# Kernel tuning notes

Hardware: AMD Instinct MI355X
Metric: run time of the kernel (lower is better)

Reference implementation:

```python
import jax, jax.numpy as jnp
import numpy as np

N_E = 1024
E_DIM = 256
BETA = 0.25
PERSISTENCE = 0.1
B, T = 16, 1024


def setup_inputs() -> dict:
    key = jax.random.key(0)
    k1, k2 = jax.random.split(key)
    z = jax.random.normal(k1, (B, T, E_DIM), dtype=jnp.float32)
    # nn.Embedding(1+n_e, e_dim) init uniform(-1/n_e, 1/n_e)
    emb_weight = jax.random.uniform(k2, (N_E + 1, E_DIM), dtype=jnp.float32,
                                    minval=-1.0 / N_E, maxval=1.0 / N_E)
    return {"z": z, "emb_weight": emb_weight}


def _loss_contrast(z, ind, book):
    # z: (B,T,e), ind: (B,T) int, book: (n_e+1, e)
    z_q = book[ind]                                   # (B,T,e)
    loss_indices = jnp.sum((z - z_q) ** 2, axis=-1)   # (B,T)
    # ||z - book||^2 expanded to avoid the (B,T,n_e+1,e) intermediate
    z_sq = jnp.sum(z * z, axis=-1)                    # (B,T)
    b_sq = jnp.sum(book * book, axis=-1)              # (n_e+1,)
    cross = jnp.einsum('bte,ne->btn', z, book)        # (B,T,n_e+1)
    loss_all = z_sq[..., None] + b_sq[None, None, :] - 2.0 * cross
    lc = jnp.maximum(loss_indices[..., None] - loss_all + 1e-6 / N_E, 0.0)
    return jnp.mean(lc)


def _forward(z, emb_weight):
    zf = z.reshape(-1, E_DIM)
    d = (jnp.sum(zf * zf, axis=1, keepdims=True)
         + jnp.sum(emb_weight * emb_weight, axis=1)
         - 2.0 * (zf @ emb_weight.T)).reshape(B, T, N_E + 1)

    ind0 = jnp.clip(jnp.argmin(d[:, 0, :], axis=1), 0, N_E - 1)  # (B,)

    def step(carry, d_t):
        ind, coe = carry                              # (B,) int, (B,) f32
        d_here = jnp.take_along_axis(d_t, ind[:, None], axis=1)[:, 0]
        ind_next = jnp.minimum(ind + 1, N_E - 1)
        d_next = jnp.take_along_axis(d_t, ind_next[:, None], axis=1)[:, 0]
        stay = d_here <= d_next - coe
        ind_new = jnp.where(stay, ind, ind_next)
        coe_new = jnp.where(stay, coe + PERSISTENCE / N_E, 0.0)
        return (ind_new, coe_new), ind_new

    coe0 = jnp.zeros((B,), jnp.float32)
    _, inds = jax.lax.scan(step, (ind0, coe0), jnp.swapaxes(d[:, 1:, :], 0, 1))
    encoding_indices = jnp.concatenate([ind0[None, :], inds], axis=0).T  # (B,T)

    book_sg = jax.lax.stop_gradient(emb_weight)  # torch uses .data/.detach() everywhere
    z_q_raw = book_sg[encoding_indices]
    z_q = z + jax.lax.stop_gradient(z_q_raw - z)  # straight-through

    # non-legacy: beta * L(z, sg(book)) + L(sg(z), sg(book))
    loss = (BETA * _loss_contrast(z, encoding_indices, book_sg)
            + _loss_contrast(jax.lax.stop_gradient(z), encoding_indices, book_sg))

    v = jnp.max(encoding_indices) - jnp.min(encoding_indices)
    return z_q, loss, encoding_indices, v


def reference(z, emb_weight):
    return _forward(z, emb_weight)
```

## Files before the change

kernel.cpp:

```cpp
#include <hip/hip_runtime.h>

#define N_E   1024
#define EDIM  256
#define BB    16
#define TT    1024
#define NROW  (BB*TT)
#define NCOL  1025
#define NPAD  1152
#define PERS  (0.1f/1024.0f)
#define EPSC  (1e-6f/1024.0f)

#define OUT_LOSS 4194304
#define OUT_IDX  4194305
#define OUT_V    4210689

#define WS_ZB   0ull
#define WS_BBF  8388608ull
#define WS_BSQ  8978432ull
#define WS_E    8983552ull
#define WS_IND  84481024ull
#define WS_PART 84546560ull

typedef __attribute__((ext_vector_type(8))) short short8;
typedef __attribute__((ext_vector_type(4))) float floatx4;

__device__ __forceinline__ unsigned short f2bf(float f) {
    unsigned int u = __float_as_uint(f);
    u = (u + 0x7fffu + ((u >> 16) & 1u)) >> 16;
    return (unsigned short)u;
}

__device__ __forceinline__ float gload_f32(const float* p) {
    float r;
    asm volatile("global_load_dword %0, %1, off" : "=v"(r) : "v"(p));
    return r;
}

__global__ __launch_bounds__(256) void k0_prep(const float* __restrict__ z,
                                               const float* __restrict__ book,
                                               unsigned short* __restrict__ zb,
                                               unsigned short* __restrict__ bb,
                                               float* __restrict__ bsq) {
    int bx = blockIdx.x, tid = threadIdx.x;
    if (bx < 4096) {
        float4 v = ((const float4*)z)[bx * 256 + tid];
        size_t o = ((size_t)bx * 256 + tid) * 4;
        zb[o + 0] = f2bf(v.x); zb[o + 1] = f2bf(v.y);
        zb[o + 2] = f2bf(v.z); zb[o + 3] = f2bf(v.w);
    } else {
        int row = bx - 4096;
        float v = (row < NCOL) ? book[(size_t)row * EDIM + tid] : 0.0f;
        bb[(size_t)row * EDIM + tid] = f2bf(v);
        __shared__ float sd[256];
        sd[tid] = v * v;
        __syncthreads();
        for (int s = 128; s > 0; s >>= 1) { if (tid < s) sd[tid] += sd[tid + s]; __syncthreads(); }
        if (tid == 0) bsq[row] = sd[0];
    }
}

__global__ __launch_bounds__(256) void k1_gemm(const unsigned short* __restrict__ zb,
                                               const unsigned short* __restrict__ bb,
                                               const float* __restrict__ bsq,
                                               float* __restrict__ e) {
    int tid = threadIdx.x;
    int lane = tid & 63, w = tid >> 6;
    int mBase = blockIdx.x * 128 + (w >> 1) * 64;
    int nBase = blockIdx.y * 128 + (w & 1) * 64;
    int r = lane & 15, q = lane >> 4;

    floatx4 acc[4][4];
    #pragma unroll
    for (int i = 0; i < 4; i++)
        #pragma unroll
        for (int j = 0; j < 4; j++) acc[i][j] = (floatx4){0.f, 0.f, 0.f, 0.f};

    const short8* A = (const short8*)zb;
    const short8* Bm = (const short8*)bb;

    #pragma unroll
    for (int ks = 0; ks < 8; ks++) {
        int k8 = ks * 4 + q;
        short8 a[4], b[4];
        #pragma unroll
        for (int i = 0; i < 4; i++) a[i] = A[(size_t)(mBase + i * 16 + r) * 32 + k8];
        #pragma unroll
        for (int j = 0; j < 4; j++) b[j] = Bm[(size_t)(nBase + j * 16 + r) * 32 + k8];
        #pragma unroll
        for (int i = 0; i < 4; i++)
            #pragma unroll
            for (int j = 0; j < 4; j++)
                acc[i][j] = __builtin_amdgcn_mfma_f32_16x16x32_bf16(a[i], b[j], acc[i][j], 0, 0, 0);
    }

    float bsql[4];
    #pragma unroll
    for (int j = 0; j < 4; j++) bsql[j] = bsq[nBase + j * 16 + r];

    #pragma unroll
    for (int i = 0; i < 4; i++)
        #pragma unroll
        for (int rr = 0; rr < 4; rr++) {
            int m = mBase + i * 16 + q * 4 + rr;
            float* erow = e + (size_t)m * NPAD;
            #pragma unroll
            for (int j = 0; j < 4; j++)
                erow[nBase + j * 16 + r] = fmaf(-2.0f, acc[i][j][rr], bsql[j]);
        }
}

__global__ __launch_bounds__(256, 1) void k2_scan(const float* __restrict__ z,
                                                  const float* __restrict__ book,
                                                  const float* __restrict__ bsq,
                                                  const float* __restrict__ e,
                                                  int* __restrict__ wind) {
    __shared__ float sb[4]; __shared__ int si[4];

    int b = blockIdx.x, tid = threadIdx.x;
    int lane = tid & 63, w = tid >> 6;

    const float4* zr = (const float4*)(z + (size_t)b * TT * EDIM);
    float4 zv = zr[lane];
    float s = zv.x * zv.x + zv.y * zv.y + zv.z * zv.z + zv.w * zv.w;
    #pragma unroll
    for (int off = 32; off; off >>= 1) s += __shfl_xor(s, off, 64);
    float zsq = s;

    float best = 3.4e38f; int bidx = 0;
    for (int wi = w; wi < 17; wi += 4) {
        int n = wi * 64 + lane;
        if (n < NCOL) {
            const float4* br = (const float4*)(book + (size_t)n * EDIM);
            float c0 = 0.f, c1 = 0.f, c2 = 0.f, c3 = 0.f;
            #pragma unroll 8
            for (int k = 0; k < 64; k++) {
                float4 bo = br[k]; float4 za = zr[k];
                c0 = fmaf(za.x, bo.x, c0); c1 = fmaf(za.y, bo.y, c1);
                c2 = fmaf(za.z, bo.z, c2); c3 = fmaf(za.w, bo.w, c3);
            }
            float cr = (c0 + c1) + (c2 + c3);
            float d0 = (zsq + bsq[n]) - 2.0f * cr;
            if (d0 < best || (d0 == best && n < bidx)) { best = d0; bidx = n; }
        }
    }
    #pragma unroll
    for (int off = 32; off; off >>= 1) {
        float ob = __shfl_xor(best, off, 64);
        int   oi = __shfl_xor(bidx, off, 64);
        if (ob < best || (ob == best && oi < bidx)) { best = ob; bidx = oi; }
    }
    if (lane == 0) { sb[w] = best; si[w] = bidx; }
    __syncthreads();
    if (w != 0) return;

    best = sb[0]; bidx = si[0];
    for (int i = 1; i < 4; i++) {
        float vv = sb[i]; int ii = si[i];
        if (vv < best || (vv == best && ii < bidx)) { best = vv; bidx = ii; }
    }

    int ind = min(bidx, N_E - 1);
    int kk = 0;
    size_t ibase = (size_t)b * TT;
    if (lane == 0) wind[ibase] = ind;

    const float* eb = e + (size_t)b * TT * NPAD;
    const float QS = 1.0f / PERS;

    float a[31];
    int   q[31];

    int cb = min(ind, 960);
    {
        #pragma unroll
        for (int j = 0; j < 31; j++)
            a[j] = gload_f32(eb + (size_t)(1 + j) * NPAD + cb + lane);
        asm volatile("s_waitcnt vmcnt(0)" ::: "memory");
        __builtin_amdgcn_sched_barrier(0);
        bool cap = (cb + lane == 1023);
        #pragma unroll
        for (int j = 0; j < 31; j++) {
            float bv = __shfl_down(a[j], 1, 64);
            int qv = (int)((bv - a[j]) * QS);
            q[j] = cap ? 0 : qv;
        }
    }

    int t = 1;
    #pragma unroll 1
    for (int c = 0; c < 33; c++) {
        int cbn = min(ind, 960);
        #pragma unroll
        for (int j = 0; j < 31; j++) {
            int tn = t + 31 + j; tn = tn < 1024 ? tn : 1023;
            a[j] = gload_f32(eb + (size_t)tn * NPAD + cbn + lane);
        }
        __builtin_amdgcn_sched_barrier(0);

        int packed = 0;
        #pragma unroll
        for (int j = 0; j < 31; j++) {
            int rel = ind - cb;
            int qv = __builtin_amdgcn_readlane(q[j], rel);
            bool stay = (kk <= qv);
            int ip1 = ind + 1; ip1 = ip1 < 1023 ? ip1 : 1023;
            ind = stay ? ind : ip1;
            kk  = stay ? kk + 1 : 0;
            packed = (lane == j) ? ind : packed;
        }
        if (lane < 31) wind[ibase + t + lane] = packed;
        __builtin_amdgcn_sched_barrier(0);

        asm volatile("s_waitcnt vmcnt(0)" ::: "memory");
        __builtin_amdgcn_sched_barrier(0);
        bool cap = (cbn + lane == 1023);
        #pragma unroll
        for (int j = 0; j < 31; j++) {
            float bv = __shfl_down(a[j], 1, 64);
            int qv = (int)((bv - a[j]) * QS);
            q[j] = cap ? 0 : qv;
        }
        cb = cbn;
        t += 31;
    }
}

__global__ __launch_bounds__(256) void k3_loss_zq(const float* __restrict__ e,
                                                  const int* __restrict__ wind,
                                                  const float* __restrict__ book,
                                                  float* __restrict__ part,
                                                  float* __restrict__ out) {
    int rIdx = blockIdx.x, tid = threadIdx.x;
    int ind = wind[rIdx];
    const float* er = e + (size_t)rIdx * NPAD;
    float eind = er[ind];
    float p = 0.0f;
    for (int n = tid; n < NCOL; n += 256) {
        float v = eind - er[n] + EPSC;
        p += v > 0.0f ? v : 0.0f;
    }
    __shared__ float sd[256];
    sd[tid] = p; __syncthreads();
    for (int s = 128; s > 0; s >>= 1) { if (tid < s) sd[tid] += sd[tid + s]; __syncthreads(); }
    if (tid == 0) { part[rIdx] = sd[0]; out[OUT_IDX + rIdx] = (float)ind; }
    out[(size_t)rIdx * 256 + tid] = book[(size_t)ind * EDIM + tid];
}

__global__ __launch_bounds__(256) void k4_final(const float* __restrict__ part,
                                                const int* __restrict__ wind,
                                                float* __restrict__ out) {
    int tid = threadIdx.x;
    float s = 0.0f;
    for (int i = tid; i < NROW; i += 256) s += part[i];
    __shared__ float sd[256];
    sd[tid] = s; __syncthreads();
    for (int st = 128; st > 0; st >>= 1) { if (tid < st) sd[tid] += sd[tid + st]; __syncthreads(); }
    if (tid == 0) {
        int mn = wind[0], mx = wind[TT - 1];
        for (int b = 1; b < BB; b++) {
            mn = min(mn, wind[(size_t)b * TT]);
            mx = max(mx, wind[(size_t)b * TT + TT - 1]);
        }
        out[OUT_LOSS] = 1.25f * sd[0] / ((float)NROW * (float)NCOL);
        out[OUT_V] = (float)(mx - mn);
    }
}

extern "C" void kernel_launch(void* const* d_in, const int* in_sizes, int n_in,
                              void* d_out, int out_size, void* d_ws, size_t ws_size,
                              hipStream_t stream) {
    const float* z    = (const float*)d_in[0];
    const float* book = (const float*)d_in[1];
    char* ws = (char*)d_ws;
    unsigned short* zb = (unsigned short*)(ws + WS_ZB);
    unsigned short* bb = (unsigned short*)(ws + WS_BBF);
    float* bsq  = (float*)(ws + WS_BSQ);
    float* e    = (float*)(ws + WS_E);
    int*   wind = (int*)(ws + WS_IND);
    float* part = (float*)(ws + WS_PART);
    float* out  = (float*)d_out;

    hipLaunchKernelGGL(k0_prep,    dim3(4096 + 1152), dim3(256), 0, stream, z, book, zb, bb, bsq);
    hipLaunchKernelGGL(k1_gemm,    dim3(128, 9),      dim3(256), 0, stream, zb, bb, bsq, e);
    hipLaunchKernelGGL(k2_scan,    dim3(16),          dim3(256), 0, stream, z, book, bsq, e, wind);
    hipLaunchKernelGGL(k3_loss_zq, dim3(16384),       dim3(256), 0, stream, e, wind, book, part, out);
    hipLaunchKernelGGL(k4_final,   dim3(1),           dim3(256), 0, stream, part, wind, out);
}
```

Baseline: 256.6 us.

## Triple-buffer scan prefetch with 15-step chunks and partial vmcnt waits

Restructures the sequential scan kernel's prefetch of distance rows from a single 31-row buffer with a full vmcnt(0) wait into three rotating 15-row register buffers. Loads are issued two chunks ahead and only the oldest batch is waited on via vmcnt(31). The aim is to hide global-load latency behind the serial index-update chain. In exchange the scan advances 15 steps per chunk, so there are more iterations, and the prefetch column base is chosen from an index that is further out of date. Correctness depends on the index not drifting more than 63 columns within the lookahead window.

```diff
diff --git a/kernel.cpp b/kernel.cpp
--- a/kernel.cpp
+++ b/kernel.cpp
@@ -109,6 +109,46 @@
         }
 }
 
+
+#define R15(X) X(0) X(1) X(2) X(3) X(4) X(5) X(6) X(7) X(8) X(9) X(10) X(11) X(12) X(13) X(14)
+
+#define DECLA(i) float A0_##i, A1_##i, A2_##i; int q_##i;
+
+#define LDR(S,i) { int _t = _tb + i; _t = _t < 1024 ? _t : 1023; \
+                   A##S##_##i = gload_f32(_pe + (size_t)_t * NPAD); }
+#define LD0(i) LDR(0,i)
+#define LD1(i) LDR(1,i)
+#define LD2(i) LDR(2,i)
+
+#define QC(S,i) { float _bv = __shfl_down(A##S##_##i, 1, 64); \
+                  int _qv = (int)((_bv - A##S##_##i) * QS); \
+                  q_##i = _capn ? 0 : _qv; }
+#define QC0(i) QC(0,i)
+#define QC1(i) QC(1,i)
+#define QC2(i) QC(2,i)
+
+#define CH(i) { int _rel = ind - cb0; \
+                int _qv = __builtin_amdgcn_readlane(q_##i, _rel); \
+                bool _stay = (kk <= _qv); \
+                int _ip1 = ind + 1; _ip1 = _ip1 < 1023 ? _ip1 : 1023; \
+                ind = _stay ? ind : _ip1; \
+                kk  = _stay ? kk + 1 : 0; \
+                packed = (lane == i) ? ind : packed; }
+
+#define ITER(SI, SC) { \
+    int cbI = ind < 960 ? ind : 960; \
+    { const float* _pe = eb + cbI + lane; int _tb = t + 45; R15(LD##SI) } \
+    __builtin_amdgcn_sched_barrier(0); \
+    int packed = 0; \
+    R15(CH) \
+    if (lane < 15 && t + lane < 1024) wind[ibase + t + lane] = packed; \
+    __builtin_amdgcn_sched_barrier(0); \
+    asm volatile("s_waitcnt vmcnt(31)" ::: "memory"); \
+    __builtin_amdgcn_sched_barrier(0); \
+    { bool _capn = (cb1 + lane == 1023); R15(QC##SC) } \
+    cb0 = cb1; cb1 = cb2; cb2 = cbI; \
+    t += 15; }
+
 __global__ __launch_bounds__(256, 1) void k2_scan(const float* __restrict__ z,
                                                   const float* __restrict__ book,
                                                   const float* __restrict__ bsq,
@@ -167,61 +207,23 @@
     const float* eb = e + (size_t)b * TT * NPAD;
     const float QS = 1.0f / PERS;
 
-    float a[31];
-    int   q[31];
-
-    int cb = min(ind, 960);
-    {
-        #pragma unroll
-        for (int j = 0; j < 31; j++)
-            a[j] = gload_f32(eb + (size_t)(1 + j) * NPAD + cb + lane);
-        asm volatile("s_waitcnt vmcnt(0)" ::: "memory");
-        __builtin_amdgcn_sched_barrier(0);
-        bool cap = (cb + lane == 1023);
-        #pragma unroll
-        for (int j = 0; j < 31; j++) {
-            float bv = __shfl_down(a[j], 1, 64);
-            int qv = (int)((bv - a[j]) * QS);
-            q[j] = cap ? 0 : qv;
-        }
-    }
+    R15(DECLA)
+
+    int cb0 = ind < 960 ? ind : 960;
+    int cb1 = cb0, cb2 = cb0;
+    { const float* _pe = eb + cb0 + lane; int _tb = 1;  R15(LD0) }
+    { const float* _pe = eb + cb1 + lane; int _tb = 16; R15(LD1) }
+    { const float* _pe = eb + cb2 + lane; int _tb = 31; R15(LD2) }
+    asm volatile("s_waitcnt vmcnt(30)" ::: "memory");
+    __builtin_amdgcn_sched_barrier(0);
+    { bool _capn = (cb0 + lane == 1023); R15(QC0) }
 
     int t = 1;
     #pragma unroll 1
-    for (int c = 0; c < 33; c++) {
-        int cbn = min(ind, 960);
-        #pragma unroll
-        for (int j = 0; j < 31; j++) {
-            int tn = t + 31 + j; tn = tn < 1024 ? tn : 1023;
-            a[j] = gload_f32(eb + (size_t)tn * NPAD + cbn + lane);
-        }
-        __builtin_amdgcn_sched_barrier(0);
-
-        int packed = 0;
-        #pragma unroll
-        for (int j = 0; j < 31; j++) {
-            int rel = ind - cb;
-            int qv = __builtin_amdgcn_readlane(q[j], rel);
-            bool stay = (kk <= qv);
-            int ip1 = ind + 1; ip1 = ip1 < 1023 ? ip1 : 1023;
-            ind = stay ? ind : ip1;
-            kk  = stay ? kk + 1 : 0;
-            packed = (lane == j) ? ind : packed;
-        }
-        if (lane < 31) wind[ibase + t + lane] = packed;
-        __builtin_amdgcn_sched_barrier(0);
-
-        asm volatile("s_waitcnt vmcnt(0)" ::: "memory");
-        __builtin_amdgcn_sched_barrier(0);
-        bool cap = (cbn + lane == 1023);
-        #pragma unroll
-        for (int j = 0; j < 31; j++) {
-            float bv = __shfl_down(a[j], 1, 64);
-            int qv = (int)((bv - a[j]) * QS);
-            q[j] = cap ? 0 : qv;
-        }
-        cb = cbn;
-        t += 31;
+    for (int cc = 0; cc < 23; cc++) {
+        ITER(0, 1)
+        ITER(1, 2)
+        ITER(2, 0)
     }
 }
 
```

Result: faster. 251.4 us (-2.0%).

## Deepen scan prefetch pipeline via global_load_lds ring buffer with smaller chunks

Applied to the files above, without the earlier changes.

Restructures the sequential scan kernel to fetch distance rows straight into an LDS ring buffer with global_load_lds. Loads are issued in chunks of 8 timesteps with 5 chunks in flight, so the data-dependent chain no longer waits on a full 31-row register batch each iteration. Each chunk's window base is tracked through a 5-deep shift register. The intent is to hide global memory latency on the serial critical path. The cost is more loop iterations, reads through LDS, and tight vmcnt bookkeeping, since prefetched windows can drift further from the current index.

```diff
diff --git a/kernel.cpp b/kernel.cpp
--- a/kernel.cpp
+++ b/kernel.cpp
@@ -28,12 +28,6 @@
     unsigned int u = __float_as_uint(f);
     u = (u + 0x7fffu + ((u >> 16) & 1u)) >> 16;
     return (unsigned short)u;
-}
-
-__device__ __forceinline__ float gload_f32(const float* p) {
-    float r;
-    asm volatile("global_load_dword %0, %1, off" : "=v"(r) : "v"(p));
-    return r;
 }
 
 __global__ __launch_bounds__(256) void k0_prep(const float* __restrict__ z,
@@ -109,12 +103,40 @@
         }
 }
 
+
+#define GCH   8
+#define DEP   5
+#define SSTR  65
+
+#define ISS(j) { int _t = ti + j; int _tc = _t < 1024 ? _t : 1023; \
+    __builtin_amdgcn_global_load_lds( \
+        (const __attribute__((address_space(1))) void*)(pE + (size_t)_tc * NPAD), \
+        (__attribute__((address_space(3))) void*)&ring[(_t & 63) * SSTR], 4, 0, 0); }
+#define ISSUE8 ISS(0) ISS(1) ISS(2) ISS(3) ISS(4) ISS(5) ISS(6) ISS(7)
+
+#define QC8(j) { int _t = tq + j; int _s = (_t & 63) * SSTR; \
+    float _A  = ring[_s + lane]; \
+    float _Bv = ring[_s + lane + 1]; \
+    int _qv = (int)((_Bv - _A) * QS); \
+    q_##j = _capn ? 0 : _qv; }
+#define QCOMP8 QC8(0) QC8(1) QC8(2) QC8(3) QC8(4) QC8(5) QC8(6) QC8(7)
+
+#define CH8(j) { int _rel = ind - b0; \
+    int _qv = __builtin_amdgcn_readlane(q_##j, _rel); \
+    bool _stay = (kk <= _qv); \
+    int _ip1 = ind + 1; _ip1 = _ip1 < 1023 ? _ip1 : 1023; \
+    ind = _stay ? ind : _ip1; \
+    kk  = _stay ? kk + 1 : 0; \
+    packed = (lane == j) ? ind : packed; }
+#define CHAIN8 CH8(0) CH8(1) CH8(2) CH8(3) CH8(4) CH8(5) CH8(6) CH8(7)
+
 __global__ __launch_bounds__(256, 1) void k2_scan(const float* __restrict__ z,
                                                   const float* __restrict__ book,
                                                   const float* __restrict__ bsq,
                                                   const float* __restrict__ e,
                                                   int* __restrict__ wind) {
     __shared__ float sb[4]; __shared__ int si[4];
+    __shared__ float ring[64 * SSTR];
 
     int b = blockIdx.x, tid = threadIdx.x;
     int lane = tid & 63, w = tid >> 6;
@@ -162,66 +184,62 @@
     int ind = min(bidx, N_E - 1);
     int kk = 0;
     size_t ibase = (size_t)b * TT;
-    if (lane == 0) wind[ibase] = ind;
 
     const float* eb = e + (size_t)b * TT * NPAD;
     const float QS = 1.0f / PERS;
 
-    float a[31];
-    int   q[31];
-
-    int cb = min(ind, 960);
+    int q_0, q_1, q_2, q_3, q_4, q_5, q_6, q_7;
+
+    asm volatile("s_waitcnt vmcnt(0)" ::: "memory");
+    __builtin_amdgcn_sched_barrier(0);
+
+    int base0 = ind < 960 ? ind : 960;
+    int b0 = base0, b1 = base0, b2 = base0, b3 = base0, b4 = base0;
+
+    #pragma unroll
+    for (int k = 0; k < DEP; k++) {
+        const float* pE = eb + base0 + lane;
+        int ti = 1 + k * GCH;
+        ISSUE8
+        if (lane == 0) *(volatile int*)(wind + ibase) = ind;
+        __builtin_amdgcn_sched_barrier(0);
+    }
+    asm volatile("s_waitcnt vmcnt(37)" ::: "memory");
+    __builtin_amdgcn_sched_barrier(0);
     {
-        #pragma unroll
-        for (int j = 0; j < 31; j++)
-            a[j] = gload_f32(eb + (size_t)(1 + j) * NPAD + cb + lane);
-        asm volatile("s_waitcnt vmcnt(0)" ::: "memory");
-        __builtin_amdgcn_sched_barrier(0);
-        bool cap = (cb + lane == 1023);
-        #pragma unroll
-        for (int j = 0; j < 31; j++) {
-            float bv = __shfl_down(a[j], 1, 64);
-            int qv = (int)((bv - a[j]) * QS);
-            q[j] = cap ? 0 : qv;
-        }
-    }
+        int tq = 1;
+        bool _capn = (b0 + lane == 1023);
+        QCOMP8
+    }
+    __builtin_amdgcn_sched_barrier(0);
 
     int t = 1;
     #pragma unroll 1
-    for (int c = 0; c < 33; c++) {
-        int cbn = min(ind, 960);
-        #pragma unroll
-        for (int j = 0; j < 31; j++) {
-            int tn = t + 31 + j; tn = tn < 1024 ? tn : 1023;
-            a[j] = gload_f32(eb + (size_t)tn * NPAD + cbn + lane);
+    for (int c = 0; c < 128; c++) {
+        int cbI = ind < 960 ? ind : 960;
+        {   const float* pE = eb + cbI + lane;
+            int ti = t + DEP * GCH;
+            ISSUE8
         }
         __builtin_amdgcn_sched_barrier(0);
 
         int packed = 0;
-        #pragma unroll
-        for (int j = 0; j < 31; j++) {
-            int rel = ind - cb;
-            int qv = __builtin_amdgcn_readlane(q[j], rel);
-            bool stay = (kk <= qv);
-            int ip1 = ind + 1; ip1 = ip1 < 1023 ? ip1 : 1023;
-            ind = stay ? ind : ip1;
-            kk  = stay ? kk + 1 : 0;
-            packed = (lane == j) ? ind : packed;
-        }
-        if (lane < 31) wind[ibase + t + lane] = packed;
-        __builtin_amdgcn_sched_barrier(0);
-
-        asm volatile("s_waitcnt vmcnt(0)" ::: "memory");
-        __builtin_amdgcn_sched_barrier(0);
-        bool cap = (cbn + lane == 1023);
-        #pragma unroll
-        for (int j = 0; j < 31; j++) {
-            float bv = __shfl_down(a[j], 1, 64);
-            int qv = (int)((bv - a[j]) * QS);
-            q[j] = cap ? 0 : qv;
-        }
-        cb = cbn;
-        t += 31;
+        CHAIN8
+        __builtin_amdgcn_sched_barrier(0);
+
+        asm volatile("s_waitcnt vmcnt(36)" ::: "memory");
+        __builtin_amdgcn_sched_barrier(0);
+
+        {
+            int tq = t + GCH;
+            bool _capn = (b1 + lane == 1023);
+            QCOMP8
+        }
+        if (lane < GCH && t + lane < 1024) wind[ibase + t + lane] = packed;
+        __builtin_amdgcn_sched_barrier(0);
+
+        b0 = b1; b1 = b2; b2 = b3; b3 = b4; b4 = cbI;
+        t += GCH;
     }
 }
 
```

Result: slower. 273.3 us (+6.5%).
